# Kernel tuning notes

Measured on AMD Instinct MI355X. Metric: run time of the kernel, lower is better.

The kernel has to match this reference:

```python
import jax, jax.numpy as jnp
import numpy as np

TEMPERATURE = 1.0
EXAGGERATION = 1.0


def setup_inputs() -> dict:
    key = jax.random.key(0)
    features = jax.random.normal(key, (8192, 128), dtype=jnp.float32)
    return {"features": features}


def _cauchy_sim(x, y):
    # 1 / ((cdist(x,y) * t)^2 + 1) == 1 / (t^2 * sq_dist + 1)
    sq = (
        jnp.sum(x * x, axis=1)[:, None]
        + jnp.sum(y * y, axis=1)[None, :]
        - 2.0 * (x @ y.T)
    )
    sq = jnp.maximum(sq, 0.0)  # numerical floor, matches cdist >= 0
    return 1.0 / (sq * (TEMPERATURE * TEMPERATURE) + 1.0)


def reference(features):
    batch_size = features.shape[0] // 2
    a = features[:batch_size]
    b = features[batch_size:]

    sim_aa = _cauchy_sim(a, a)  # [B, B]
    sim_bb = _cauchy_sim(b, b)  # [B, B]
    sim_ab = _cauchy_sim(a, b)  # [B, B]

    tempered_alignment = jnp.mean(jnp.log(jnp.diagonal(sim_ab)))

    self_mask = jnp.eye(batch_size, dtype=bool)
    sim_aa = jnp.where(self_mask, 0.0, sim_aa)
    sim_bb = jnp.where(self_mask, 0.0, sim_bb)

    # hstack((sim_ab.T, sim_bb)).sum(1) == sim_ab.sum(0) + sim_bb.sum(1)
    logsumexp_1 = jnp.mean(jnp.log(jnp.sum(sim_ab, axis=0) + jnp.sum(sim_bb, axis=1)))
    logsumexp_2 = jnp.mean(jnp.log(jnp.sum(sim_aa, axis=1) + jnp.sum(sim_ab, axis=1)))
    raw_uniformity = logsumexp_1 + logsumexp_2

    loss = -(EXAGGERATION * tempered_alignment - raw_uniformity / 2.0)
    return loss
```

## Files before the change

kernel.cpp:

```cpp
#include <hip/hip_runtime.h>
#include <hip/hip_bf16.h>

typedef __bf16 bf16x8 __attribute__((ext_vector_type(8)));
typedef float  f32x4  __attribute__((ext_vector_type(4)));

static constexpr int D     = 128;
static constexpr int BATCH = 4096;
static constexpr int N     = 8192;
static constexpr int BT    = 128;
static constexpr int NT    = N / BT;
static constexpr int TRI   = NT * (NT + 1) / 2;

__global__ __launch_bounds__(256) void prep_kernel(const float* __restrict__ f,
                                                   unsigned short* __restrict__ Fpack,
                                                   float* __restrict__ norms,
                                                   float* __restrict__ diag,
                                                   float* __restrict__ out) {
    if (blockIdx.x == 0 && threadIdx.x == 0) out[0] = 0.f;
    const int w = threadIdx.x >> 6, lane = threadIdx.x & 63;
    const int i = blockIdx.x * 4 + w;
    const float2 va = *(const float2*)(f + (size_t)i * D + lane * 2);
    const float2 vb = *(const float2*)(f + (size_t)(i + BATCH) * D + lane * 2);
    union { __bf16 h[2]; unsigned int u; } pa, pb;
    pa.h[0] = (__bf16)va.x; pa.h[1] = (__bf16)va.y;
    pb.h[0] = (__bf16)vb.x; pb.h[1] = (__bf16)vb.y;

    const int c   = lane >> 2;
    const int off = (lane & 3) * 4;
    auto storeF = [&](int row, unsigned int bits) {
        char* p = (char*)Fpack + (size_t)(row >> 7) * 32768 + ((row >> 5) & 3) * 8192
                + (c >> 2) * 2048 + ((row >> 4) & 1) * 1024 + (c & 3) * 256 + (row & 15) * 16 + off;
        *(unsigned int*)p = bits;
    };
    storeF(i, pa.u);
    storeF(i + BATCH, pb.u);

    float na = va.x * va.x + va.y * va.y;
    float nb = vb.x * vb.x + vb.y * vb.y;
    const float dx = va.x - vb.x, dy = va.y - vb.y;
    float dd = dx * dx + dy * dy;
    #pragma unroll
    for (int m = 1; m <= 32; m <<= 1) {
        na += __shfl_xor(na, m); nb += __shfl_xor(nb, m); dd += __shfl_xor(dd, m);
    }
    if (lane == 0) {
        norms[i] = na; norms[i + BATCH] = nb;
        diag[i] = 1.f / (dd + 1.f);
    }
}

__global__ __launch_bounds__(256, 4) void tile_kernel(const unsigned short* __restrict__ Fpack,
                                                      const float* __restrict__ norms,
                                                      float* __restrict__ P) {
    const int bid = blockIdx.x;
    const int id = (bid & 7) * (TRI / 8) + (bid >> 3);
    int ti = (int)((sqrtf(8.f * (float)id + 1.f) - 1.f) * 0.5f);
    while ((ti + 1) * (ti + 2) / 2 <= id) ++ti;
    while (ti * (ti + 1) / 2 > id) --ti;
    const int tj = id - ti * (ti + 1) / 2;
    const bool diagblk = (ti == tj);

    __shared__ float colbuf[BT];

    const int tid = threadIdx.x, wv = tid >> 6, lane = tid & 63;
    const int lr = lane & 15, hk = lane >> 4;
    if (tid < BT) colbuf[tid] = 0.f;
    __syncthreads();

    const char* Ab = (const char*)Fpack + (size_t)ti * 32768 + wv * 8192;
    const char* Bb = (const char*)Fpack + (size_t)tj * 32768;
    const int lo = hk * 256 + lr * 16;

    f32x4 acc[2][8];
    #pragma unroll
    for (int i = 0; i < 2; ++i)
        #pragma unroll
        for (int j = 0; j < 8; ++j)
            acc[i][j] = (f32x4){0.f, 0.f, 0.f, 0.f};

    #pragma unroll
    for (int ks = 0; ks < 4; ++ks) {
        bf16x8 av[2], bv[8];
        av[0] = *(const bf16x8*)(Ab + ks * 2048 + lo);
        av[1] = *(const bf16x8*)(Ab + ks * 2048 + 1024 + lo);
        #pragma unroll
        for (int fj = 0; fj < 8; ++fj)
            bv[fj] = *(const bf16x8*)(Bb + (fj >> 1) * 8192 + ks * 2048 + (fj & 1) * 1024 + lo);
        #pragma unroll
        for (int fj = 0; fj < 8; ++fj) {
            acc[0][fj] = __builtin_amdgcn_mfma_f32_16x16x32_bf16(av[0], bv[fj], acc[0][fj], 0, 0, 0);
            acc[1][fj] = __builtin_amdgcn_mfma_f32_16x16x32_bf16(av[1], bv[fj], acc[1][fj], 0, 0, 0);
        }
    }

    float colN[8];
    #pragma unroll
    for (int fj = 0; fj < 8; ++fj)
        colN[fj] = norms[tj * BT + fj * 16 + lr];

    float* PR = P + ((size_t)ti * NT + tj) * BT;
    #pragma unroll
    for (int fi = 0; fi < 2; ++fi) {
        const int lrow = wv * 32 + fi * 16 + hk * 4;
        const f32x4 rN = *(const f32x4*)(norms + ti * BT + lrow);
        f32x4 rs = (f32x4){0.f, 0.f, 0.f, 0.f};
        #pragma unroll
        for (int fj = 0; fj < 8; ++fj) {
            const int lcol = fj * 16 + lr;
            #pragma unroll
            for (int r = 0; r < 4; ++r) {
                float sq = rN[r] + colN[fj] - 2.f * acc[fi][fj][r];
                sq = fmaxf(sq, 0.f);
                float sim = __builtin_amdgcn_rcpf(sq + 1.f);
                if (diagblk && (lrow + r == lcol)) sim = 0.f;
                rs[r] += sim;
                acc[fi][fj][r] = sim;
            }
        }
        #pragma unroll
        for (int r = 0; r < 4; ++r) {
            rs[r] += __shfl_xor(rs[r], 1);
            rs[r] += __shfl_xor(rs[r], 2);
            rs[r] += __shfl_xor(rs[r], 4);
            rs[r] += __shfl_xor(rs[r], 8);
        }
        if (lr == 0)
            *(f32x4*)(PR + lrow) = rs;
    }

    if (!diagblk) {
        #pragma unroll
        for (int fj = 0; fj < 8; ++fj) {
            float cs = 0.f;
            #pragma unroll
            for (int fi = 0; fi < 2; ++fi)
                #pragma unroll
                for (int r = 0; r < 4; ++r)
                    cs += acc[fi][fj][r];
            cs += __shfl_xor(cs, 16);
            cs += __shfl_xor(cs, 32);
            if (hk == 0)
                atomicAdd(&colbuf[fj * 16 + lr], cs);
        }
        __syncthreads();
        if (tid < BT)
            P[((size_t)tj * NT + ti) * BT + tid] = colbuf[tid];
    }
}

__global__ __launch_bounds__(128) void finalize_kernel(const float* __restrict__ P,
                                                       const float* __restrict__ diag,
                                                       float* __restrict__ out) {
    const int t = blockIdx.x;
    const int r = threadIdx.x;
    const float* base = P + (size_t)t * NT * BT + r;
    float s = 0.f;
    #pragma unroll 8
    for (int k = 0; k < NT; ++k) s += base[k * BT];
    const int i = t * BT + r;
    float term = 0.5f * __logf(s);
    if (i >= BATCH) term -= __logf(diag[i - BATCH]);
    #pragma unroll
    for (int m = 1; m <= 32; m <<= 1) term += __shfl_xor(term, m);
    if ((threadIdx.x & 63) == 0)
        atomicAdd(out, term / (float)BATCH);
}

extern "C" void kernel_launch(void* const* d_in, const int* in_sizes, int n_in,
                              void* d_out, int out_size, void* d_ws, size_t ws_size,
                              hipStream_t stream) {
    const float* feat = (const float*)d_in[0];
    char* ws = (char*)d_ws;
    unsigned short* Fpack = (unsigned short*)ws;
    float* norms = (float*)(ws + (2u << 20));
    float* diag  = (float*)(ws + (2u << 20) + 32768);
    float* P     = (float*)(ws + (2u << 20) + 49152);
    float* out   = (float*)d_out;

    prep_kernel<<<BATCH / 4, 256, 0, stream>>>(feat, Fpack, norms, diag, out);
    tile_kernel<<<TRI, 256, 0, stream>>>(Fpack, norms, P);
    finalize_kernel<<<NT, 128, 0, stream>>>(P, diag, out);
}
```

Baseline: 95.46 us.

## Switch Gram tiles to FP8 scaled MFMA with async LDS staging

Features are now quantized to FP8 e4m3 in a row-major, XOR-swizzled layout instead of packed BF16. The tile kernel stages the A and B tiles into shared memory with global_load_lds and runs the 16x16x128 f8f6f4 scaled MFMA with unit scales, so each fragment needs one MFMA instead of four. This halves the bytes read and cuts matrix instruction count. The cost is lower precision in the distance computation, where norms stay FP32 but dot products use e4m3, and it adds 32KB of LDS per block, which may limit occupancy.

Result: faster. 78.72 us (-17.5%).

```diff
diff --git a/kernel.cpp b/kernel.cpp
--- a/kernel.cpp
+++ b/kernel.cpp
@@ -1,8 +1,10 @@
 #include <hip/hip_runtime.h>
 #include <hip/hip_bf16.h>
-
-typedef __bf16 bf16x8 __attribute__((ext_vector_type(8)));
-typedef float  f32x4  __attribute__((ext_vector_type(4)));
+#include <hip/hip_fp8.h>
+
+typedef float f32x4 __attribute__((ext_vector_type(4)));
+typedef int   i32x4 __attribute__((ext_vector_type(4)));
+typedef int   i32x8 __attribute__((ext_vector_type(8)));
 
 static constexpr int D     = 128;
 static constexpr int BATCH = 4096;
@@ -10,9 +12,16 @@
 static constexpr int BT    = 128;
 static constexpr int NT    = N / BT;
 static constexpr int TRI   = NT * (NT + 1) / 2;
+static constexpr int SCALE1 = 0x7F7F7F7F;
+
+__device__ __forceinline__ void load_lds16(const void* g, void* l) {
+    __builtin_amdgcn_global_load_lds(
+        (const __attribute__((address_space(1))) unsigned int*)g,
+        (__attribute__((address_space(3))) unsigned int*)l, 16, 0, 0);
+}
 
 __global__ __launch_bounds__(256) void prep_kernel(const float* __restrict__ f,
-                                                   unsigned short* __restrict__ Fpack,
+                                                   unsigned char* __restrict__ Fp8,
                                                    float* __restrict__ norms,
                                                    float* __restrict__ diag,
                                                    float* __restrict__ out) {
@@ -21,19 +30,17 @@
     const int i = blockIdx.x * 4 + w;
     const float2 va = *(const float2*)(f + (size_t)i * D + lane * 2);
     const float2 vb = *(const float2*)(f + (size_t)(i + BATCH) * D + lane * 2);
-    union { __bf16 h[2]; unsigned int u; } pa, pb;
-    pa.h[0] = (__bf16)va.x; pa.h[1] = (__bf16)va.y;
-    pb.h[0] = (__bf16)vb.x; pb.h[1] = (__bf16)vb.y;
-
-    const int c   = lane >> 2;
-    const int off = (lane & 3) * 4;
-    auto storeF = [&](int row, unsigned int bits) {
-        char* p = (char*)Fpack + (size_t)(row >> 7) * 32768 + ((row >> 5) & 3) * 8192
-                + (c >> 2) * 2048 + ((row >> 4) & 1) * 1024 + (c & 3) * 256 + (row & 15) * 16 + off;
-        *(unsigned int*)p = bits;
+
+    auto storeF = [&](int row, float x, float y) {
+        union { unsigned char b[2]; unsigned short u; } pk;
+        pk.b[0] = __hip_fp8_e4m3(x).__x;
+        pk.b[1] = __hip_fp8_e4m3(y).__x;
+        const size_t dst = (size_t)(row >> 7) * 16384 + (row & 127) * 128
+                         + (((lane >> 3) ^ (row & 7)) << 4) + (lane & 7) * 2;
+        *(unsigned short*)(Fp8 + dst) = pk.u;
     };
-    storeF(i, pa.u);
-    storeF(i + BATCH, pb.u);
+    storeF(i, va.x, va.y);
+    storeF(i + BATCH, vb.x, vb.y);
 
     float na = va.x * va.x + va.y * va.y;
     float nb = vb.x * vb.x + vb.y * vb.y;
@@ -49,7 +56,7 @@
     }
 }
 
-__global__ __launch_bounds__(256, 4) void tile_kernel(const unsigned short* __restrict__ Fpack,
+__global__ __launch_bounds__(256, 4) void tile_kernel(const unsigned char* __restrict__ Fp8,
                                                       const float* __restrict__ norms,
                                                       float* __restrict__ P) {
     const int bid = blockIdx.x;
@@ -60,16 +67,30 @@
     const int tj = id - ti * (ti + 1) / 2;
     const bool diagblk = (ti == tj);
 
+    __shared__ __align__(16) unsigned char As[16384];
+    __shared__ __align__(16) unsigned char Bs[16384];
     __shared__ float colbuf[BT];
 
     const int tid = threadIdx.x, wv = tid >> 6, lane = tid & 63;
     const int lr = lane & 15, hk = lane >> 4;
     if (tid < BT) colbuf[tid] = 0.f;
+
+    const unsigned char* Aimg = Fp8 + (size_t)ti * 16384;
+    const unsigned char* Bimg = Fp8 + (size_t)tj * 16384;
+    #pragma unroll
+    for (int it = 0; it < 4; ++it)
+        load_lds16(Aimg + (it * 256 + tid) * 16, As + it * 4096 + wv * 1024);
+    #pragma unroll
+    for (int it = 0; it < 4; ++it)
+        load_lds16(Bimg + (it * 256 + tid) * 16, Bs + it * 4096 + wv * 1024);
     __syncthreads();
 
-    const char* Ab = (const char*)Fpack + (size_t)ti * 32768 + wv * 8192;
-    const char* Bb = (const char*)Fpack + (size_t)tj * 32768;
-    const int lo = hk * 256 + lr * 16;
+    auto frag = [&](const unsigned char* S, int rowbase) -> i32x8 {
+        const int row = rowbase + lr;
+        const i32x4 q0 = *(const i32x4*)(S + row * 128 + (((hk * 2 + 0) ^ (lr & 7)) << 4));
+        const i32x4 q1 = *(const i32x4*)(S + row * 128 + (((hk * 2 + 1) ^ (lr & 7)) << 4));
+        return __builtin_shufflevector(q0, q1, 0, 1, 2, 3, 4, 5, 6, 7);
+    };
 
     f32x4 acc[2][8];
     #pragma unroll
@@ -78,19 +99,15 @@
         for (int j = 0; j < 8; ++j)
             acc[i][j] = (f32x4){0.f, 0.f, 0.f, 0.f};
 
-    #pragma unroll
-    for (int ks = 0; ks < 4; ++ks) {
-        bf16x8 av[2], bv[8];
-        av[0] = *(const bf16x8*)(Ab + ks * 2048 + lo);
-        av[1] = *(const bf16x8*)(Ab + ks * 2048 + 1024 + lo);
-        #pragma unroll
-        for (int fj = 0; fj < 8; ++fj)
-            bv[fj] = *(const bf16x8*)(Bb + (fj >> 1) * 8192 + ks * 2048 + (fj & 1) * 1024 + lo);
-        #pragma unroll
-        for (int fj = 0; fj < 8; ++fj) {
-            acc[0][fj] = __builtin_amdgcn_mfma_f32_16x16x32_bf16(av[0], bv[fj], acc[0][fj], 0, 0, 0);
-            acc[1][fj] = __builtin_amdgcn_mfma_f32_16x16x32_bf16(av[1], bv[fj], acc[1][fj], 0, 0, 0);
-        }
+    const i32x8 av0 = frag(As, wv * 32);
+    const i32x8 av1 = frag(As, wv * 32 + 16);
+    #pragma unroll
+    for (int fj = 0; fj < 8; ++fj) {
+        const i32x8 bv = frag(Bs, fj * 16);
+        acc[0][fj] = __builtin_amdgcn_mfma_scale_f32_16x16x128_f8f6f4(
+            av0, bv, acc[0][fj], 0, 0, 0, SCALE1, 0, SCALE1);
+        acc[1][fj] = __builtin_amdgcn_mfma_scale_f32_16x16x128_f8f6f4(
+            av1, bv, acc[1][fj], 0, 0, 0, SCALE1, 0, SCALE1);
     }
 
     float colN[8];
@@ -171,13 +188,13 @@
                               hipStream_t stream) {
     const float* feat = (const float*)d_in[0];
     char* ws = (char*)d_ws;
-    unsigned short* Fpack = (unsigned short*)ws;
-    float* norms = (float*)(ws + (2u << 20));
-    float* diag  = (float*)(ws + (2u << 20) + 32768);
-    float* P     = (float*)(ws + (2u << 20) + 49152);
+    unsigned char* Fp8 = (unsigned char*)ws;
+    float* norms = (float*)(ws + (1u << 20));
+    float* diag  = (float*)(ws + (1u << 20) + 32768);
+    float* P     = (float*)(ws + (1u << 20) + 49152);
     float* out   = (float*)d_out;
 
-    prep_kernel<<<BATCH / 4, 256, 0, stream>>>(feat, Fpack, norms, diag, out);
-    tile_kernel<<<TRI, 256, 0, stream>>>(Fpack, norms, P);
+    prep_kernel<<<BATCH / 4, 256, 0, stream>>>(feat, Fp8, norms, diag, out);
+    tile_kernel<<<TRI, 256, 0, stream>>>(Fp8, norms, P);
     finalize_kernel<<<NT, 128, 0, stream>>>(P, diag, out);
 }
```
